# Kernel optimization log

Measured on AMD Instinct MI355X. Metric: run time of the kernel, lower is better.

Reference implementation:

```python
import jax, jax.numpy as jnp
import numpy as np
import math

B, N, F0, HID, OUT, K = 8, 2048, 128, 64, 16, 10


def setup_inputs() -> dict:
    key = jax.random.key(0)
    ks = jax.random.split(key, 6)
    X = jax.random.normal(ks[0], (B, N, F0), dtype=jnp.float32)
    # Row-stochastic dense 'rescaled Laplacian': spectrum inside unit disk,
    # so K-th order Bernstein polynomial stays numerically stable.
    A = jax.random.uniform(ks[1], (N, N), dtype=jnp.float32)
    L = A / jnp.sum(A, axis=1, keepdims=True)
    W1 = jax.random.normal(ks[2], (F0, HID), dtype=jnp.float32) / np.float32(np.sqrt(F0))
    b1 = jnp.zeros((HID,), dtype=jnp.float32)
    W2 = jax.random.normal(ks[3], (HID, OUT), dtype=jnp.float32) / np.float32(np.sqrt(HID))
    b2 = jnp.zeros((OUT,), dtype=jnp.float32)
    theta = 0.02 * jax.random.normal(ks[4], (K + 1,), dtype=jnp.float32)
    return {"X": X, "L": L, "W1": W1, "b1": b1, "W2": W2, "b2": b2,
            "theta": theta, "dp": 0}


def _bern_filter(Hf, L, theta, binom):
    # g(L) Hf = sum_i theta_i C(K,i) L^i (I-L)^{K-i} Hf
    # Computed by applying L / (I-L) directly to the (B,N,F) features
    # (mathematically identical to forming the NxN basis matrices).
    Lap = lambda Y: jnp.einsum('vw,bwf->bvf', L, Y)
    ys = [Hf]                       # ys[k] = (I-L)^k Hf
    for _ in range(K):
        ys.append(ys[-1] - Lap(ys[-1]))
    a = theta * binom               # (K+1,)
    # Horner in L: r = a_K Hf; r <- L r + a_i (I-L)^{K-i} Hf
    r = a[K] * Hf
    for i in range(K - 1, -1, -1):
        r = Lap(r) + a[i] * ys[K - i]
    return r


def reference(X, L, W1, b1, W2, b2, theta, dp):
    binom = jnp.asarray([math.comb(K, i) for i in range(K + 1)], dtype=X.dtype)
    # dropout with p=dp=0 is identity
    Hf = jax.nn.relu(X @ W1 + b1)          # (B, N, HID)
    Hf = _bern_filter(Hf, L, theta, binom) # (B, N, HID)
    Hg = jnp.mean(Hf, axis=1)              # (B, HID)
    logits = Hg @ W2 + b2                  # (B, OUT)
    return logits
```

## Files before the change

kernel.cpp:

```cpp
#include <hip/hip_runtime.h>

#define NN     2048
#define F0D    128
#define HIDD   64
#define OUTD   16
#define KDEG   10
#define NCHAIN 128
#define COLS   16

typedef unsigned int u32;

#define CTAG(j) (0xC0DE0000u + (u32)(j))
#define HTAG    0xBEEF0001u

static __device__ __forceinline__ u32 ld_flag(const u32* p) {
    return __hip_atomic_load(p, __ATOMIC_RELAXED, __HIP_MEMORY_SCOPE_AGENT);
}
static __device__ __forceinline__ void st_flag(u32* p, u32 v) {
    __hip_atomic_store(p, v, __ATOMIC_RELAXED, __HIP_MEMORY_SCOPE_AGENT);
}
static __device__ __forceinline__ void st_data(float* p, float v) {
    __hip_atomic_store(p, v, __ATOMIC_RELAXED, __HIP_MEMORY_SCOPE_AGENT);
}

__global__ __launch_bounds__(256, 1) void k_fused(
    const float* __restrict__ X, const float* __restrict__ L,
    const float* __restrict__ W1, const float* __restrict__ b1,
    const float* __restrict__ W2, const float* __restrict__ b2,
    const float* __restrict__ theta, float* __restrict__ out,
    float* __restrict__ ws)
{
    float* PB  = ws;
    u32*   FLH = (u32*)(ws + 49152);
    float* HP  = ws + 51200;

    __shared__ union {
        struct { float Lt[NN * COLS]; float redf[4][16]; float cbv[16]; int rdy[16]; } mv;
        struct { float W1t[64][132]; float redm[16][65]; float wv[64]; } hd;
    } sm;

    const int g = blockIdx.x;
    const int t = threadIdx.x;

    if (g < NCHAIN) {
        const int u0 = g * COLS;

        if (t <= KDEG) {
            const float C10[11] = {1,10,45,120,210,252,210,120,45,10,1};
            float acc = 0.f;
            for (int i = 0; i <= t; ++i) {
                int n = KDEG - i, r = t - i;
                long long cm = 1;
                for (int s = 1; s <= r; ++s) cm = cm * (n - r + s) / s;
                float term = theta[i] * C10[i] * (float)cm;
                if ((t - i) & 1) term = -term;
                acc += term;
            }
            sm.mv.cbv[t] = acc;
        }
        if (t < 16) sm.mv.rdy[t] = 0;

        const float4* L4  = (const float4*)L;
        float4*       Lt4 = (float4*)sm.mv.Lt;
        const int qc = t & 3, r0 = t >> 2;
        {
            float4 acc = make_float4(0.f, 0.f, 0.f, 0.f);
            #pragma unroll 8
            for (int i = 0; i < 32; ++i) {
                int v = r0 + 64 * i;
                float4 lv = L4[(size_t)v * (NN / 4) + (u0 >> 2) + qc];
                Lt4[v * 4 + qc] = lv;
                acc.x += lv.x; acc.y += lv.y; acc.z += lv.z; acc.w += lv.w;
            }
            #pragma unroll
            for (int m = 4; m <= 32; m <<= 1) {
                acc.x += __shfl_xor(acc.x, m); acc.y += __shfl_xor(acc.y, m);
                acc.z += __shfl_xor(acc.z, m); acc.w += __shfl_xor(acc.w, m);
            }
            int lane = t & 63, wid = t >> 6;
            if (lane < 4) *(float4*)&sm.mv.redf[wid][lane * 4] = acc;
        }
        __syncthreads();

        float val = 0.f, wacc = 0.f;
        if (t < COLS) {
            float s = sm.mv.redf[0][t] + sm.mv.redf[1][t]
                    + sm.mv.redf[2][t] + sm.mv.redf[3][t];
            val = s; wacc = sm.mv.cbv[0];
            st_data(&PB[u0 + t], s);
        }
        if (t < 64) {
            asm volatile("s_waitcnt vmcnt(0)" ::: "memory");
            if (t == 0) st_flag(((u32*)(ws + 28672)) + g * 16, CTAG(1));
        }

        for (int j = 2; j <= KDEG; ++j) {
            if (t < 64) {
                const u32* fb = (const u32*)(ws + 28672 + (size_t)(j - 2) * 2048);
                const u32 tag = CTAG(j - 1);
                const u32* f0 = fb + t * 16;
                const u32* f1 = fb + (t + 64) * 16;
                while (!__all(ld_flag(f0) == tag && ld_flag(f1) == tag))
                    __builtin_amdgcn_s_sleep(1);
                asm volatile("" ::: "memory");
                if (t == 0) ((volatile int*)sm.mv.rdy)[j] = 1;
            } else {
                volatile int* vr = (volatile int*)sm.mv.rdy;
                while (vr[j] == 0) __builtin_amdgcn_s_sleep(1);
                asm volatile("" ::: "memory");
            }

            const float* psrc = PB + (size_t)(j - 2) * 2048;
            float4 a2 = make_float4(0.f, 0.f, 0.f, 0.f);
            #pragma unroll 8
            for (int k = 0; k < 32; ++k) {
                int v = r0 + 64 * k;
                float xv = psrc[v];
                float4 lv = Lt4[v * 4 + qc];
                a2.x += lv.x * xv; a2.y += lv.y * xv;
                a2.z += lv.z * xv; a2.w += lv.w * xv;
            }
            #pragma unroll
            for (int m = 4; m <= 32; m <<= 1) {
                a2.x += __shfl_xor(a2.x, m); a2.y += __shfl_xor(a2.y, m);
                a2.z += __shfl_xor(a2.z, m); a2.w += __shfl_xor(a2.w, m);
            }
            {
                int lane = t & 63, wid = t >> 6;
                if (lane < 4) *(float4*)&sm.mv.redf[wid][lane * 4] = a2;
            }
            __syncthreads();

            if (t < COLS) {
                float s = sm.mv.redf[0][t] + sm.mv.redf[1][t]
                        + sm.mv.redf[2][t] + sm.mv.redf[3][t];
                wacc += sm.mv.cbv[j - 1] * val;
                val = s;
                float outv = (j < KDEG) ? s : (wacc + sm.mv.cbv[KDEG] * s);
                st_data(&PB[(size_t)(j - 1) * 2048 + u0 + t], outv);
            }
            if (t < 64) {
                asm volatile("s_waitcnt vmcnt(0)" ::: "memory");
                if (t == 0)
                    st_flag(((u32*)(ws + 28672 + (size_t)(j - 1) * 2048)) + g * 16,
                            CTAG(j));
            }
        }

        if (g == 0) {
            if (t < 32) {
                u32 need = 0xFu;
                while (need) {
                    #pragma unroll
                    for (int i = 0; i < 4; ++i)
                        if (need & (1u << i))
                            if (ld_flag(FLH + (t + 32 * i) * 16) == HTAG)
                                need &= ~(1u << i);
                    if (need) __builtin_amdgcn_s_sleep(2);
                }
                asm volatile("" ::: "memory");
            }
            __syncthreads();
            float s2[2];
            #pragma unroll
            for (int e = 0; e < 2; ++e) {
                int idx = t * 2 + e, b = idx >> 6, h = idx & 63;
                const float* hp = HP + (size_t)(b * 32) * 64 + h;
                float ss = 0.f;
                #pragma unroll
                for (int vc = 0; vc < 32; ++vc) ss += hp[vc * 64];
                s2[e] = ss;
            }
            sm.mv.Lt[t * 2]     = s2[0];
            sm.mv.Lt[t * 2 + 1] = s2[1];
            __syncthreads();
            if (t < 128) {
                int o = t & 15, bb = t >> 4;
                float a3 = b2[o];
                #pragma unroll
                for (int h = 0; h < HIDD; ++h)
                    a3 += sm.mv.Lt[bb * 64 + h] * W2[h * 16 + o];
                out[bb * 16 + o] = a3;
            }
        }
        return;
    }

    const int u = g - NCHAIN;
    const int vchunk = u & 31, bA = u >> 5, bB = bA + 4;

    if (t == 0) {
        const u32* fp = ((const u32*)(ws + 28672)) + u * 16;
        while (ld_flag(fp) != CTAG(1)) __builtin_amdgcn_s_sleep(2);
    }
    __syncthreads();

    for (int i = t; i < F0D * HIDD; i += 256) {
        int f = i >> 6, h = i & 63;
        sm.hd.W1t[h][f] = W1[i];
    }
    __syncthreads();

    const int hg = t & 15, vg = t >> 4;
    const int vbase = vchunk * 64 + vg * 4;
    const float* XA = X + ((size_t)bA * NN + vbase) * F0D;
    const float* XB = X + ((size_t)bB * NN + vbase) * F0D;
    float accA[4][4] = {}, accB[4][4] = {};
    for (int f = 0; f < F0D; f += 4) {
        float4 xa[4], xb[4];
        #pragma unroll
        for (int i = 0; i < 4; ++i) {
            xa[i] = *(const float4*)(XA + (size_t)i * F0D + f);
            xb[i] = *(const float4*)(XB + (size_t)i * F0D + f);
        }
        #pragma unroll
        for (int jj = 0; jj < 4; ++jj) {
            float4 wr = *(const float4*)(&sm.hd.W1t[hg + 16 * jj][f]);
            #pragma unroll
            for (int i = 0; i < 4; ++i) {
                accA[i][jj] += xa[i].x * wr.x + xa[i].y * wr.y
                             + xa[i].z * wr.z + xa[i].w * wr.w;
                accB[i][jj] += xb[i].x * wr.x + xb[i].y * wr.y
                             + xb[i].z * wr.z + xb[i].w * wr.w;
            }
        }
    }

    if (t < 4) {
        const u32* fp = ((u32*)(ws + 28672 + (size_t)(KDEG - 1) * 2048))
                      + (vchunk * 4 + t) * 16;
        while (ld_flag(fp) != CTAG(KDEG)) __builtin_amdgcn_s_sleep(2);
        asm volatile("" ::: "memory");
    }
    __syncthreads();
    if (t < 16)
        ((float4*)sm.hd.wv)[t] =
            ((const float4*)(PB + (size_t)(KDEG - 1) * 2048 + vchunk * 64))[t];
    __syncthreads();

    const float inv = 1.0f / (float)NN;
    float hsA[4] = {0.f,0.f,0.f,0.f}, hsB[4] = {0.f,0.f,0.f,0.f};
    #pragma unroll
    for (int i = 0; i < 4; ++i) {
        float we = sm.hd.wv[vg * 4 + i];
        #pragma unroll
        for (int jj = 0; jj < 4; ++jj) {
            float rA = accA[i][jj] + b1[hg + 16 * jj];
            float rB = accB[i][jj] + b1[hg + 16 * jj];
            rA = rA > 0.f ? rA : 0.f;
            rB = rB > 0.f ? rB : 0.f;
            hsA[jj] += rA * we;
            hsB[jj] += rB * we;
        }
    }
    #pragma unroll
    for (int jj = 0; jj < 4; ++jj) sm.hd.redm[vg][hg + 16 * jj] = hsA[jj];
    __syncthreads();
    if (t < 64) {
        float s = 0.f;
        #pragma unroll
        for (int i = 0; i < 16; ++i) s += sm.hd.redm[i][t];
        st_data(&HP[(size_t)(bA * 32 + vchunk) * 64 + t], s * inv);
    }
    __syncthreads();
    #pragma unroll
    for (int jj = 0; jj < 4; ++jj) sm.hd.redm[vg][hg + 16 * jj] = hsB[jj];
    __syncthreads();
    if (t < 64) {
        float s = 0.f;
        #pragma unroll
        for (int i = 0; i < 16; ++i) s += sm.hd.redm[i][t];
        st_data(&HP[(size_t)(bB * 32 + vchunk) * 64 + t], s * inv);
    }
    if (t < 64) {
        asm volatile("s_waitcnt vmcnt(0)" ::: "memory");
        if (t == 0) st_flag(FLH + u * 16, HTAG);
    }
}

extern "C" void kernel_launch(void* const* d_in, const int* in_sizes, int n_in,
                              void* d_out, int out_size, void* d_ws, size_t ws_size,
                              hipStream_t stream) {
    const float* X     = (const float*)d_in[0];
    const float* L     = (const float*)d_in[1];
    const float* W1    = (const float*)d_in[2];
    const float* b1    = (const float*)d_in[3];
    const float* W2    = (const float*)d_in[4];
    const float* b2    = (const float*)d_in[5];
    const float* theta = (const float*)d_in[6];
    float* outp = (float*)d_out;
    float* wsp  = (float*)d_ws;

    hipLaunchKernelGGL(k_fused, dim3(256), dim3(256), 0, stream,
                       X, L, W1, b1, W2, b2, theta, outp, wsp);
}
```

Baseline: 123.4 us.

## Make each wavefront own its columns and sync per-wave instead of per-block

```diff
diff --git a/kernel.cpp b/kernel.cpp
--- a/kernel.cpp
+++ b/kernel.cpp
@@ -21,6 +21,9 @@
 }
 static __device__ __forceinline__ void st_data(float* p, float v) {
     __hip_atomic_store(p, v, __ATOMIC_RELAXED, __HIP_MEMORY_SCOPE_AGENT);
+}
+static __device__ __forceinline__ float ld_f32ag(const float* p) {
+    return __hip_atomic_load(p, __ATOMIC_RELAXED, __HIP_MEMORY_SCOPE_AGENT);
 }
 
 __global__ __launch_bounds__(256, 1) void k_fused(
@@ -31,19 +34,22 @@
     float* __restrict__ ws)
 {
     float* PB  = ws;
-    u32*   FLH = (u32*)(ws + 49152);
-    float* HP  = ws + 51200;
+    u32*   FLH = (u32*)(ws + 147456);
+    float* Hg  = ws + 149504;
 
     __shared__ union {
-        struct { float Lt[NN * COLS]; float redf[4][16]; float cbv[16]; int rdy[16]; } mv;
+        struct { float Lt[NN * COLS]; float redf[4][16]; float cbv[16]; } mv;
         struct { float W1t[64][132]; float redm[16][65]; float wv[64]; } hd;
     } sm;
 
-    const int g = blockIdx.x;
-    const int t = threadIdx.x;
+    const int g    = blockIdx.x;
+    const int t    = threadIdx.x;
+    const int w    = t >> 6;
+    const int lane = t & 63;
 
     if (g < NCHAIN) {
-        const int u0 = g * COLS;
+        const int u0  = g * COLS;
+        const int wid = g * 4 + w;
 
         if (t <= KDEG) {
             const float C10[11] = {1,10,45,120,210,252,210,120,45,10,1};
@@ -58,128 +64,113 @@
             }
             sm.mv.cbv[t] = acc;
         }
-        if (t < 16) sm.mv.rdy[t] = 0;
 
         const float4* L4  = (const float4*)L;
         float4*       Lt4 = (float4*)sm.mv.Lt;
         const int qc = t & 3, r0 = t >> 2;
         {
-            float4 acc = make_float4(0.f, 0.f, 0.f, 0.f);
+            float4 a = make_float4(0.f, 0.f, 0.f, 0.f);
             #pragma unroll 8
             for (int i = 0; i < 32; ++i) {
                 int v = r0 + 64 * i;
                 float4 lv = L4[(size_t)v * (NN / 4) + (u0 >> 2) + qc];
-                Lt4[v * 4 + qc] = lv;
-                acc.x += lv.x; acc.y += lv.y; acc.z += lv.z; acc.w += lv.w;
+                Lt4[qc * 2048 + v] = lv;
+                a.x += lv.x; a.y += lv.y; a.z += lv.z; a.w += lv.w;
             }
             #pragma unroll
             for (int m = 4; m <= 32; m <<= 1) {
-                acc.x += __shfl_xor(acc.x, m); acc.y += __shfl_xor(acc.y, m);
-                acc.z += __shfl_xor(acc.z, m); acc.w += __shfl_xor(acc.w, m);
-            }
-            int lane = t & 63, wid = t >> 6;
-            if (lane < 4) *(float4*)&sm.mv.redf[wid][lane * 4] = acc;
+                a.x += __shfl_xor(a.x, m); a.y += __shfl_xor(a.y, m);
+                a.z += __shfl_xor(a.z, m); a.w += __shfl_xor(a.w, m);
+            }
+            if (lane < 4) *(float4*)&sm.mv.redf[w][lane * 4] = a;
         }
         __syncthreads();
 
-        float val = 0.f, wacc = 0.f;
-        if (t < COLS) {
-            float s = sm.mv.redf[0][t] + sm.mv.redf[1][t]
-                    + sm.mv.redf[2][t] + sm.mv.redf[3][t];
-            val = s; wacc = sm.mv.cbv[0];
-            st_data(&PB[u0 + t], s);
-        }
-        if (t < 64) {
-            asm volatile("s_waitcnt vmcnt(0)" ::: "memory");
-            if (t == 0) st_flag(((u32*)(ws + 28672)) + g * 16, CTAG(1));
-        }
+        float vx = sm.mv.redf[0][4*w+0] + sm.mv.redf[1][4*w+0]
+                 + sm.mv.redf[2][4*w+0] + sm.mv.redf[3][4*w+0];
+        float vy = sm.mv.redf[0][4*w+1] + sm.mv.redf[1][4*w+1]
+                 + sm.mv.redf[2][4*w+1] + sm.mv.redf[3][4*w+1];
+        float vz = sm.mv.redf[0][4*w+2] + sm.mv.redf[1][4*w+2]
+                 + sm.mv.redf[2][4*w+2] + sm.mv.redf[3][4*w+2];
+        float vw = sm.mv.redf[0][4*w+3] + sm.mv.redf[1][4*w+3]
+                 + sm.mv.redf[2][4*w+3] + sm.mv.redf[3][4*w+3];
+        float c0 = sm.mv.cbv[0];
+        float wx = c0, wy = c0, wz = c0, ww = c0;
+
+        if (lane == 0) {
+            st_data(&PB[u0 + 4*w + 0], vx); st_data(&PB[u0 + 4*w + 1], vy);
+            st_data(&PB[u0 + 4*w + 2], vz); st_data(&PB[u0 + 4*w + 3], vw);
+        }
+        asm volatile("s_waitcnt vmcnt(0)" ::: "memory");
+        if (lane == 0) st_flag(((u32*)(ws + 65536)) + wid * 16, CTAG(1));
 
         for (int j = 2; j <= KDEG; ++j) {
-            if (t < 64) {
-                const u32* fb = (const u32*)(ws + 28672 + (size_t)(j - 2) * 2048);
+            {
+                const u32* fb = (const u32*)(ws + 65536 + (size_t)(j - 2) * 8192);
                 const u32 tag = CTAG(j - 1);
-                const u32* f0 = fb + t * 16;
-                const u32* f1 = fb + (t + 64) * 16;
-                while (!__all(ld_flag(f0) == tag && ld_flag(f1) == tag))
+                for (;;) {
+                    int ok = 1;
+                    #pragma unroll
+                    for (int i = 0; i < 8; ++i)
+                        ok &= (ld_flag(fb + (lane + 64 * i) * 16) == tag);
+                    if (__all(ok)) break;
                     __builtin_amdgcn_s_sleep(1);
+                }
                 asm volatile("" ::: "memory");
-                if (t == 0) ((volatile int*)sm.mv.rdy)[j] = 1;
-            } else {
-                volatile int* vr = (volatile int*)sm.mv.rdy;
-                while (vr[j] == 0) __builtin_amdgcn_s_sleep(1);
-                asm volatile("" ::: "memory");
-            }
-
+            }
             const float* psrc = PB + (size_t)(j - 2) * 2048;
-            float4 a2 = make_float4(0.f, 0.f, 0.f, 0.f);
+            float ax = 0.f, ay = 0.f, az = 0.f, aw = 0.f;
             #pragma unroll 8
             for (int k = 0; k < 32; ++k) {
-                int v = r0 + 64 * k;
+                int v = lane + 64 * k;
                 float xv = psrc[v];
-                float4 lv = Lt4[v * 4 + qc];
-                a2.x += lv.x * xv; a2.y += lv.y * xv;
-                a2.z += lv.z * xv; a2.w += lv.w * xv;
+                float4 lv = Lt4[w * 2048 + v];
+                ax += lv.x * xv; ay += lv.y * xv;
+                az += lv.z * xv; aw += lv.w * xv;
             }
             #pragma unroll
-            for (int m = 4; m <= 32; m <<= 1) {
-                a2.x += __shfl_xor(a2.x, m); a2.y += __shfl_xor(a2.y, m);
-                a2.z += __shfl_xor(a2.z, m); a2.w += __shfl_xor(a2.w, m);
-            }
-            {
-                int lane = t & 63, wid = t >> 6;
-                if (lane < 4) *(float4*)&sm.mv.redf[wid][lane * 4] = a2;
-            }
+            for (int m = 1; m <= 32; m <<= 1) {
+                ax += __shfl_xor(ax, m); ay += __shfl_xor(ay, m);
+                az += __shfl_xor(az, m); aw += __shfl_xor(aw, m);
+            }
+            float cj = sm.mv.cbv[j - 1];
+            wx += cj * vx; wy += cj * vy; wz += cj * vz; ww += cj * vw;
+            vx = ax; vy = ay; vz = az; vw = aw;
+            float ox = vx, oy = vy, oz = vz, ow = vw;
+            if (j == KDEG) {
+                float cK = sm.mv.cbv[KDEG];
+                ox = wx + cK * vx; oy = wy + cK * vy;
+                oz = wz + cK * vz; ow = ww + cK * vw;
+            }
+            float* dst = PB + (size_t)(j - 1) * 2048 + u0 + 4 * w;
+            if (lane == 0) {
+                st_data(dst + 0, ox); st_data(dst + 1, oy);
+                st_data(dst + 2, oz); st_data(dst + 3, ow);
+            }
+            asm volatile("s_waitcnt vmcnt(0)" ::: "memory");
+            if (lane == 0)
+                st_flag(((u32*)(ws + 65536 + (size_t)(j - 1) * 8192)) + wid * 16,
+                        CTAG(j));
+        }
+
+        if (g == 0) {
             __syncthreads();
-
-            if (t < COLS) {
-                float s = sm.mv.redf[0][t] + sm.mv.redf[1][t]
-                        + sm.mv.redf[2][t] + sm.mv.redf[3][t];
-                wacc += sm.mv.cbv[j - 1] * val;
-                val = s;
-                float outv = (j < KDEG) ? s : (wacc + sm.mv.cbv[KDEG] * s);
-                st_data(&PB[(size_t)(j - 1) * 2048 + u0 + t], outv);
-            }
             if (t < 64) {
-                asm volatile("s_waitcnt vmcnt(0)" ::: "memory");
-                if (t == 0)
-                    st_flag(((u32*)(ws + 28672 + (size_t)(j - 1) * 2048)) + g * 16,
-                            CTAG(j));
-            }
-        }
-
-        if (g == 0) {
-            if (t < 32) {
-                u32 need = 0xFu;
-                while (need) {
-                    #pragma unroll
-                    for (int i = 0; i < 4; ++i)
-                        if (need & (1u << i))
-                            if (ld_flag(FLH + (t + 32 * i) * 16) == HTAG)
-                                need &= ~(1u << i);
-                    if (need) __builtin_amdgcn_s_sleep(2);
+                for (;;) {
+                    int ok = (ld_flag(FLH + t * 16) == HTAG)
+                           & (ld_flag(FLH + (t + 64) * 16) == HTAG);
+                    if (__all(ok)) break;
+                    __builtin_amdgcn_s_sleep(2);
                 }
                 asm volatile("" ::: "memory");
             }
-            __syncthreads();
-            float s2[2];
-            #pragma unroll
-            for (int e = 0; e < 2; ++e) {
-                int idx = t * 2 + e, b = idx >> 6, h = idx & 63;
-                const float* hp = HP + (size_t)(b * 32) * 64 + h;
-                float ss = 0.f;
-                #pragma unroll
-                for (int vc = 0; vc < 32; ++vc) ss += hp[vc * 64];
-                s2[e] = ss;
-            }
-            sm.mv.Lt[t * 2]     = s2[0];
-            sm.mv.Lt[t * 2 + 1] = s2[1];
             __syncthreads();
             if (t < 128) {
                 int o = t & 15, bb = t >> 4;
                 float a3 = b2[o];
                 #pragma unroll
                 for (int h = 0; h < HIDD; ++h)
-                    a3 += sm.mv.Lt[bb * 64 + h] * W2[h * 16 + o];
+                    a3 += ld_f32ag(&Hg[bb * 64 + h]) * W2[h * 16 + o];
                 out[bb * 16 + o] = a3;
             }
         }
@@ -190,7 +181,7 @@
     const int vchunk = u & 31, bA = u >> 5, bB = bA + 4;
 
     if (t == 0) {
-        const u32* fp = ((const u32*)(ws + 28672)) + u * 16;
+        const u32* fp = ((const u32*)(ws + 65536)) + (u * 4) * 16;
         while (ld_flag(fp) != CTAG(1)) __builtin_amdgcn_s_sleep(2);
     }
     __syncthreads();
@@ -226,9 +217,9 @@
         }
     }
 
-    if (t < 4) {
-        const u32* fp = ((u32*)(ws + 28672 + (size_t)(KDEG - 1) * 2048))
-                      + (vchunk * 4 + t) * 16;
+    if (t < 16) {
+        const u32* fp = ((const u32*)(ws + 65536 + (size_t)(KDEG - 1) * 8192))
+                      + (vchunk * 16 + t) * 16;
         while (ld_flag(fp) != CTAG(KDEG)) __builtin_amdgcn_s_sleep(2);
         asm volatile("" ::: "memory");
     }
@@ -260,7 +251,7 @@
         float s = 0.f;
         #pragma unroll
         for (int i = 0; i < 16; ++i) s += sm.hd.redm[i][t];
-        st_data(&HP[(size_t)(bA * 32 + vchunk) * 64 + t], s * inv);
+        atomicAdd(&Hg[bA * 64 + t], s * inv);
     }
     __syncthreads();
     #pragma unroll
@@ -270,12 +261,10 @@
         float s = 0.f;
         #pragma unroll
         for (int i = 0; i < 16; ++i) s += sm.hd.redm[i][t];
-        st_data(&HP[(size_t)(bB * 32 + vchunk) * 64 + t], s * inv);
-    }
-    if (t < 64) {
-        asm volatile("s_waitcnt vmcnt(0)" ::: "memory");
-        if (t == 0) st_flag(FLH + u * 16, HTAG);
-    }
+        atomicAdd(&Hg[bB * 64 + t], s * inv);
+    }
+    asm volatile("s_waitcnt vmcnt(0)" ::: "memory");
+    if (t == 0) st_flag(FLH + u * 16, HTAG);
 }
 
 extern "C" void kernel_launch(void* const* d_in, const int* in_sizes, int n_in,
@@ -291,6 +280,8 @@
     float* outp = (float*)d_out;
     float* wsp  = (float*)d_ws;
 
+    hipMemsetAsync((char*)d_ws + 147456 * sizeof(float), 0, 10240, stream);
+
     hipLaunchKernelGGL(k_fused, dim3(256), dim3(256), 0, stream,
                        X, L, W1, b1, W2, b2, theta, outp, wsp);
 }
```

Measured after the change: 149.6 us. +21.2%, slower.
